# Kernel optimization log

Hardware: AMD Instinct MI355X
Metric: run time of the kernel (lower is better)

## Reference

```python
import jax, jax.numpy as jnp
import numpy as np

B, S, N, D = 8, 1024, 128, 256
LN_EPS = 1e-5
NEG = -10000.0


def setup_inputs() -> dict:
    key = jax.random.key(0)
    ks = jax.random.split(key, 6)
    doc_state = jax.random.normal(ks[0], (B, S, D), dtype=jnp.float32)
    # binary node->token membership mask (batch, nodes, seq)
    nodes_mapping = (jax.random.uniform(ks[1], (B, N, S)) < 0.25).astype(jnp.float32)
    nodes_len = jnp.sum(nodes_mapping, axis=-1).astype(jnp.int32)  # unused by forward, kept for signature parity
    # attention MLP params: Linear(D,D) -> LayerNorm(D) -> GELU -> Linear(D,1)
    W1 = jax.random.normal(ks[2], (D, D), dtype=jnp.float32) / np.float32(np.sqrt(D))
    b1 = jnp.zeros((D,), jnp.float32)
    gamma = jnp.ones((D,), jnp.float32)
    beta = jnp.zeros((D,), jnp.float32)
    W2 = jax.random.normal(ks[3], (D, 1), dtype=jnp.float32) / np.float32(np.sqrt(D))
    b2 = jnp.zeros((1,), jnp.float32)
    return {"doc_state": doc_state, "nodes_mapping": nodes_mapping, "nodes_len": nodes_len,
            "W1": W1, "b1": b1, "gamma": gamma, "beta": beta, "W2": W2, "b2": b2}


def reference(doc_state, nodes_mapping, nodes_len, W1, b1, gamma, beta, W2, b2):
    # scorer MLP: (B,S,D) -> (B,S)
    h = doc_state @ W1 + b1
    mu = jnp.mean(h, axis=-1, keepdims=True)
    var = jnp.mean(jnp.square(h - mu), axis=-1, keepdims=True)
    h = (h - mu) * jax.lax.rsqrt(var + LN_EPS) * gamma + beta
    h = jax.nn.gelu(h, approximate=False)  # torch GELU default = erf form
    scores = (h @ W2 + b2)[..., 0]  # (B, S)
    # masked logits over tokens per node: mapping * score + (1-mapping)*(-1e4)
    logits = nodes_mapping * scores[:, None, :] + (1.0 - nodes_mapping) * NEG  # (B,N,S)
    attn = jax.nn.softmax(logits, axis=2)  # softmax over seq dim
    # pooled = sum_s mapping * attn * doc_state, without materializing (B,N,S,D)
    pooled = jnp.einsum('bns,bns,bsd->bnd', nodes_mapping, attn, doc_state)
    return pooled
```

## Files before the change

### kernel.cpp

```cpp
#include <hip/hip_runtime.h>
#include <hip/hip_bf16.h>
#include <math.h>

#define DD 256
#define SS 1024
#define BB 8
#define NN 128
#define TOK 16
#define KC 64
#define NT 8
#define SC 8
#define SCH (SS/SC)

__global__ __launch_bounds__(256) void scorer_kernel(
    const float* __restrict__ doc, const float* __restrict__ W1,
    const float* __restrict__ b1, const float* __restrict__ gamma,
    const float* __restrict__ beta, const float* __restrict__ W2,
    const float* __restrict__ b2, float* __restrict__ scores)
{
    __shared__ float xs[TOK][DD];
    __shared__ float w1s[KC][DD];

    const int tid  = threadIdx.x;
    const int wave = tid >> 6, lane = tid & 63;
    const int t0   = blockIdx.x * TOK;
    const int c0   = lane * 4;

    {
        const float4* src = reinterpret_cast<const float4*>(doc + (size_t)t0 * DD);
        float4* dst = reinterpret_cast<float4*>(&xs[0][0]);
#pragma unroll
        for (int r = 0; r < 4; ++r) dst[tid + 256 * r] = src[tid + 256 * r];
    }

    float4 acc[4];
    {
        const float4 bv = *reinterpret_cast<const float4*>(b1 + c0);
#pragma unroll
        for (int t = 0; t < 4; ++t) acc[t] = bv;
    }
    const float* xw = &xs[wave * 4][0];

    for (int kc = 0; kc < DD / KC; ++kc) {
        __syncthreads();
        {
            const float4* wsrc = reinterpret_cast<const float4*>(W1 + (size_t)kc * KC * DD);
            float4* wdst = reinterpret_cast<float4*>(&w1s[0][0]);
#pragma unroll
            for (int r = 0; r < 16; ++r) wdst[tid + 256 * r] = wsrc[tid + 256 * r];
        }
        __syncthreads();
#pragma unroll 4
        for (int k4 = 0; k4 < KC / 4; ++k4) {
            const int kb = k4 * 4;
            const float4 w0 = *reinterpret_cast<const float4*>(&w1s[kb + 0][c0]);
            const float4 w1 = *reinterpret_cast<const float4*>(&w1s[kb + 1][c0]);
            const float4 w2 = *reinterpret_cast<const float4*>(&w1s[kb + 2][c0]);
            const float4 w3 = *reinterpret_cast<const float4*>(&w1s[kb + 3][c0]);
#pragma unroll
            for (int t = 0; t < 4; ++t) {
                const float4 xv = *reinterpret_cast<const float4*>(xw + (size_t)t * DD + kc * KC + kb);
                acc[t].x = fmaf(xv.x, w0.x, acc[t].x);
                acc[t].y = fmaf(xv.x, w0.y, acc[t].y);
                acc[t].z = fmaf(xv.x, w0.z, acc[t].z);
                acc[t].w = fmaf(xv.x, w0.w, acc[t].w);
                acc[t].x = fmaf(xv.y, w1.x, acc[t].x);
                acc[t].y = fmaf(xv.y, w1.y, acc[t].y);
                acc[t].z = fmaf(xv.y, w1.z, acc[t].z);
                acc[t].w = fmaf(xv.y, w1.w, acc[t].w);
                acc[t].x = fmaf(xv.z, w2.x, acc[t].x);
                acc[t].y = fmaf(xv.z, w2.y, acc[t].y);
                acc[t].z = fmaf(xv.z, w2.z, acc[t].z);
                acc[t].w = fmaf(xv.z, w2.w, acc[t].w);
                acc[t].x = fmaf(xv.w, w3.x, acc[t].x);
                acc[t].y = fmaf(xv.w, w3.y, acc[t].y);
                acc[t].z = fmaf(xv.w, w3.z, acc[t].z);
                acc[t].w = fmaf(xv.w, w3.w, acc[t].w);
            }
        }
    }

    const float4 gm = *reinterpret_cast<const float4*>(gamma + c0);
    const float4 be = *reinterpret_cast<const float4*>(beta + c0);
    const float4 w2v = *reinterpret_cast<const float4*>(W2 + c0);
    const float b2v = b2[0];

#pragma unroll
    for (int t = 0; t < 4; ++t) {
        float s1 = acc[t].x + acc[t].y + acc[t].z + acc[t].w;
        float s2 = acc[t].x * acc[t].x + acc[t].y * acc[t].y
                 + acc[t].z * acc[t].z + acc[t].w * acc[t].w;
#pragma unroll
        for (int off = 32; off > 0; off >>= 1) {
            s1 += __shfl_xor(s1, off, 64);
            s2 += __shfl_xor(s2, off, 64);
        }
        const float mean = s1 * (1.f / DD);
        const float var  = s2 * (1.f / DD) - mean * mean;
        const float inv  = rsqrtf(var + 1e-5f);
        float n0 = (acc[t].x - mean) * inv * gm.x + be.x;
        float n1 = (acc[t].y - mean) * inv * gm.y + be.y;
        float n2 = (acc[t].z - mean) * inv * gm.z + be.z;
        float n3 = (acc[t].w - mean) * inv * gm.w + be.w;
        const float kq = 0.70710678118654752f;
        float g0 = 0.5f * n0 * (1.f + erff(n0 * kq));
        float g1 = 0.5f * n1 * (1.f + erff(n1 * kq));
        float g2 = 0.5f * n2 * (1.f + erff(n2 * kq));
        float g3 = 0.5f * n3 * (1.f + erff(n3 * kq));
        float sc = g0 * w2v.x + g1 * w2v.y + g2 * w2v.z + g3 * w2v.w;
#pragma unroll
        for (int off = 32; off > 0; off >>= 1) sc += __shfl_xor(sc, off, 64);
        if (lane == 0) scores[t0 + wave * 4 + t] = sc + b2v;
    }
}

__global__ __launch_bounds__(256) void pool_e_kernel(
    const float* __restrict__ doc, const float* __restrict__ mapping,
    const float* __restrict__ scores, float* __restrict__ part,
    float* __restrict__ zpart)
{
    __shared__ float w_lds[NT][SCH];
    __shared__ float z_s[NT];

    const int blk   = blockIdx.x;
    const int c     = blk % SC;
    const int bt    = blk / SC;
    const int ntile = bt & 15;
    const int b     = bt >> 4;
    const int s0    = c * SCH;
    const int tid = threadIdx.x, wave = tid >> 6, lane = tid & 63;

    {
        const int nl = wave * 2 + (lane >> 5);
        const int g  = b * NN + ntile * NT + nl;
        const float4 mp = reinterpret_cast<const float4*>(mapping + (size_t)g * SS + s0)[lane & 31];
        const float4 sv = reinterpret_cast<const float4*>(scores + (size_t)b * SS + s0)[lane & 31];
        float4 e;
        e.x = (mp.x > 0.5f) ? __expf(sv.x) : 0.f;
        e.y = (mp.y > 0.5f) ? __expf(sv.y) : 0.f;
        e.z = (mp.z > 0.5f) ? __expf(sv.z) : 0.f;
        e.w = (mp.w > 0.5f) ? __expf(sv.w) : 0.f;
        reinterpret_cast<float4*>(&w_lds[nl][0])[lane & 31] = e;
        float z = e.x + e.y + e.z + e.w;
#pragma unroll
        for (int off = 16; off > 0; off >>= 1) z += __shfl_xor(z, off, 64);
        if ((lane & 31) == 0) z_s[nl] = z;
    }
    __syncthreads();

    float acc[NT];
#pragma unroll
    for (int n = 0; n < NT; ++n) acc[n] = 0.f;
    const float* docb = doc + ((size_t)b * SS + s0) * DD;

    float d0 = docb[(size_t)0 * DD + tid], d1 = docb[(size_t)1 * DD + tid];
    float d2 = docb[(size_t)2 * DD + tid], d3 = docb[(size_t)3 * DD + tid];
    for (int s4 = 0; s4 < SCH - 4; s4 += 4) {
        const float n0 = docb[(size_t)(s4 + 4) * DD + tid];
        const float n1 = docb[(size_t)(s4 + 5) * DD + tid];
        const float n2 = docb[(size_t)(s4 + 6) * DD + tid];
        const float n3 = docb[(size_t)(s4 + 7) * DD + tid];
#pragma unroll
        for (int n = 0; n < NT; ++n) {
            const float4 wv = *reinterpret_cast<const float4*>(&w_lds[n][s4]);
            acc[n] = fmaf(wv.x, d0, acc[n]);
            acc[n] = fmaf(wv.y, d1, acc[n]);
            acc[n] = fmaf(wv.z, d2, acc[n]);
            acc[n] = fmaf(wv.w, d3, acc[n]);
        }
        d0 = n0; d1 = n1; d2 = n2; d3 = n3;
    }
    {
        const int s4 = SCH - 4;
#pragma unroll
        for (int n = 0; n < NT; ++n) {
            const float4 wv = *reinterpret_cast<const float4*>(&w_lds[n][s4]);
            acc[n] = fmaf(wv.x, d0, acc[n]);
            acc[n] = fmaf(wv.y, d1, acc[n]);
            acc[n] = fmaf(wv.z, d2, acc[n]);
            acc[n] = fmaf(wv.w, d3, acc[n]);
        }
    }

    float* p = part + (size_t)blk * (NT * DD);
#pragma unroll
    for (int n = 0; n < NT; ++n) p[(size_t)n * DD + tid] = acc[n];
    if (tid < NT) zpart[(size_t)blk * NT + tid] = z_s[tid];
}

__global__ __launch_bounds__(256) void reduce_div_kernel(
    const float* __restrict__ part, const float* __restrict__ zpart,
    float* __restrict__ out)
{
    const int o = blockIdx.x * 256 + threadIdx.x;
    const int d = o & 255;
    const int g = o >> 8;
    const int b = g >> 7;
    const int n = g & 127;
    const int ntile = n >> 3, nl = n & 7;
    const int bp0 = (b * 16 + ntile) * SC;
    float s = 0.f, z = 0.f;
#pragma unroll
    for (int c = 0; c < SC; ++c) {
        const int bp = bp0 + c;
        s += part[(size_t)bp * (NT * DD) + (size_t)nl * DD + d];
        z += zpart[(size_t)bp * NT + nl];
    }
    out[o] = (z > 0.f) ? (s / z) : 0.f;
}

__global__ __launch_bounds__(256) void stats_kernel(
    const float* __restrict__ mapping, const float* __restrict__ scores,
    float* __restrict__ mx_out, float* __restrict__ invz_out)
{
    __shared__ float sc_s[SS];
    const int tid = threadIdx.x, wave = tid >> 6, lane = tid & 63;
    const int g0 = blockIdx.x * 4;
    const int b  = g0 >> 7;

    reinterpret_cast<float4*>(sc_s)[tid] =
        reinterpret_cast<const float4*>(scores + (size_t)b * SS)[tid];
    __syncthreads();

    const int g = g0 + wave;
    const float4* mrow4 = reinterpret_cast<const float4*>(mapping + (size_t)g * SS);
    const float4* sc4   = reinterpret_cast<const float4*>(sc_s);

    float4 mv[4], sv[4];
    float mx = -INFINITY;
#pragma unroll
    for (int q = 0; q < 4; ++q) {
        mv[q] = mrow4[lane + (q << 6)];
        sv[q] = sc4[lane + (q << 6)];
        if (mv[q].x > 0.5f) mx = fmaxf(mx, sv[q].x);
        if (mv[q].y > 0.5f) mx = fmaxf(mx, sv[q].y);
        if (mv[q].z > 0.5f) mx = fmaxf(mx, sv[q].z);
        if (mv[q].w > 0.5f) mx = fmaxf(mx, sv[q].w);
    }
#pragma unroll
    for (int off = 32; off > 0; off >>= 1) mx = fmaxf(mx, __shfl_xor(mx, off, 64));
    float z = 0.f;
#pragma unroll
    for (int q = 0; q < 4; ++q) {
        if (mv[q].x > 0.5f) z += __expf(sv[q].x - mx);
        if (mv[q].y > 0.5f) z += __expf(sv[q].y - mx);
        if (mv[q].z > 0.5f) z += __expf(sv[q].z - mx);
        if (mv[q].w > 0.5f) z += __expf(sv[q].w - mx);
    }
#pragma unroll
    for (int off = 32; off > 0; off >>= 1) z += __shfl_xor(z, off, 64);
    if (lane == 0) {
        mx_out[g]   = mx;
        invz_out[g] = (z > 0.f) ? (1.f / z) : 0.f;
    }
}

__global__ __launch_bounds__(256) void pool_direct_kernel(
    const float* __restrict__ doc, const float* __restrict__ mapping,
    const float* __restrict__ scores, const float* __restrict__ mx_in,
    const float* __restrict__ invz_in, float* __restrict__ out)
{
    __shared__ float w_lds[8][SS];

    const int bt    = blockIdx.x;
    const int ntile = bt & 15;
    const int b     = bt >> 4;
    const int tid = threadIdx.x, wave = tid >> 6, lane = tid & 63;

    {
        const int nl = wave * 2 + (lane >> 5);
        const int g  = b * NN + ntile * 8 + nl;
        const float mx   = mx_in[g];
        const float invz = invz_in[g];
        const float4* mrow4 = reinterpret_cast<const float4*>(mapping + (size_t)g * SS);
        const float4* srow4 = reinterpret_cast<const float4*>(scores + (size_t)b * SS);
        float4* wrow4 = reinterpret_cast<float4*>(&w_lds[nl][0]);
        const int idx0 = lane & 31;
#pragma unroll
        for (int q = 0; q < SS / 128; ++q) {
            const int idx = idx0 + 32 * q;
            const float4 mp = mrow4[idx];
            const float4 sv = srow4[idx];
            float4 e;
            e.x = (mp.x > 0.5f) ? __expf(sv.x - mx) * invz : 0.f;
            e.y = (mp.y > 0.5f) ? __expf(sv.y - mx) * invz : 0.f;
            e.z = (mp.z > 0.5f) ? __expf(sv.z - mx) * invz : 0.f;
            e.w = (mp.w > 0.5f) ? __expf(sv.w - mx) * invz : 0.f;
            wrow4[idx] = e;
        }
    }
    __syncthreads();

    float acc[8];
#pragma unroll
    for (int n = 0; n < 8; ++n) acc[n] = 0.f;
    const float* docb = doc + (size_t)b * SS * DD;

    for (int s4 = 0; s4 < SS; s4 += 4) {
        const float d0 = docb[(size_t)(s4 + 0) * DD + tid];
        const float d1 = docb[(size_t)(s4 + 1) * DD + tid];
        const float d2 = docb[(size_t)(s4 + 2) * DD + tid];
        const float d3 = docb[(size_t)(s4 + 3) * DD + tid];
#pragma unroll
        for (int n = 0; n < 8; ++n) {
            const float4 wv = *reinterpret_cast<const float4*>(&w_lds[n][s4]);
            acc[n] = fmaf(wv.x, d0, acc[n]);
            acc[n] = fmaf(wv.y, d1, acc[n]);
            acc[n] = fmaf(wv.z, d2, acc[n]);
            acc[n] = fmaf(wv.w, d3, acc[n]);
        }
    }

    float* outb = out + (((size_t)b * NN) + (size_t)ntile * 8) * DD;
#pragma unroll
    for (int n = 0; n < 8; ++n) outb[(size_t)n * DD + tid] = acc[n];
}

extern "C" void kernel_launch(void* const* d_in, const int* in_sizes, int n_in,
                              void* d_out, int out_size, void* d_ws, size_t ws_size,
                              hipStream_t stream) {
    const float* doc     = (const float*)d_in[0];
    const float* mapping = (const float*)d_in[1];
    const float* W1    = (const float*)d_in[3];
    const float* b1    = (const float*)d_in[4];
    const float* gamma = (const float*)d_in[5];
    const float* beta  = (const float*)d_in[6];
    const float* W2    = (const float*)d_in[7];
    const float* b2    = (const float*)d_in[8];
    float* out = (float*)d_out;

    char* base = (char*)d_ws;
    size_t off = 0;
    float* scores = (float*)(base + off); off += (size_t)BB * SS * 4;
    float* part   = (float*)(base + off); off += (size_t)BB * 16 * SC * NT * DD * 4;
    float* zpart  = (float*)(base + off); off += (size_t)BB * 16 * SC * NT * 4;
    const size_t need = off;

    scorer_kernel<<<BB * SS / TOK, 256, 0, stream>>>(doc, W1, b1, gamma, beta, W2, b2, scores);

    if (ws_size >= need) {
        pool_e_kernel<<<BB * 16 * SC, 256, 0, stream>>>(doc, mapping, scores, part, zpart);
        reduce_div_kernel<<<(BB * NN * DD) / 256, 256, 0, stream>>>(part, zpart, out);
    } else {
        float* mx   = scores + BB * SS;
        float* invz = mx + BB * NN;
        stats_kernel<<<(BB * NN) / 4, 256, 0, stream>>>(mapping, scores, mx, invz);
        pool_direct_kernel<<<BB * 16, 256, 0, stream>>>(doc, mapping, scores, mx, invz, out);
    }
}
```

Baseline: 53.27 us.

## Compute scorer Linear on MFMA with split-bf16 three-term emulation of fp32

Replaces the fp32 FMA scorer GEMM with a bf16 MFMA kernel that splits each operand into hi and lo bf16 parts and sums three products to approximate fp32 accuracy. W1 is transposed and split by a small prep kernel. The LayerNorm, GELU and W2 epilogue moves into a separate combine kernel that reads an 8 MB h buffer from global memory. This adds two launches and an extra round trip of the full hidden activation through memory. The fallback path for a small workspace now needs more space, and the smallest case no longer launches anything.

```diff
diff --git a/kernel.cpp b/kernel.cpp
--- a/kernel.cpp
+++ b/kernel.cpp
@@ -11,6 +11,242 @@
 #define NT 8
 #define SC 8
 #define SCH (SS/SC)
+
+typedef __attribute__((ext_vector_type(8))) short short8;
+typedef __attribute__((ext_vector_type(4))) float f32x4;
+
+__device__ __forceinline__ unsigned short f2bf(float x) {
+    unsigned u = __builtin_bit_cast(unsigned, x);
+    u += 0x7fffu + ((u >> 16) & 1u);
+    return (unsigned short)(u >> 16);
+}
+__device__ __forceinline__ float bf2f(unsigned short h) {
+    return __builtin_bit_cast(float, (unsigned)h << 16);
+}
+__device__ __forceinline__ void cvt8(const float* __restrict__ p, short8& hi, short8& lo) {
+    const float4 xa = *reinterpret_cast<const float4*>(p);
+    const float4 xb = *reinterpret_cast<const float4*>(p + 4);
+    unsigned short h;
+    h = f2bf(xa.x); hi[0] = (short)h; lo[0] = (short)f2bf(xa.x - bf2f(h));
+    h = f2bf(xa.y); hi[1] = (short)h; lo[1] = (short)f2bf(xa.y - bf2f(h));
+    h = f2bf(xa.z); hi[2] = (short)h; lo[2] = (short)f2bf(xa.z - bf2f(h));
+    h = f2bf(xa.w); hi[3] = (short)h; lo[3] = (short)f2bf(xa.w - bf2f(h));
+    h = f2bf(xb.x); hi[4] = (short)h; lo[4] = (short)f2bf(xb.x - bf2f(h));
+    h = f2bf(xb.y); hi[5] = (short)h; lo[5] = (short)f2bf(xb.y - bf2f(h));
+    h = f2bf(xb.z); hi[6] = (short)h; lo[6] = (short)f2bf(xb.z - bf2f(h));
+    h = f2bf(xb.w); hi[7] = (short)h; lo[7] = (short)f2bf(xb.w - bf2f(h));
+}
+
+__global__ __launch_bounds__(256) void split_w1t_kernel(
+    const float* __restrict__ W1,
+    unsigned short* __restrict__ w1t_hi, unsigned short* __restrict__ w1t_lo)
+{
+    __shared__ float tl[64][65];
+    const int tid = threadIdx.x;
+    const int k0 = (blockIdx.x >> 2) * 64, n0 = (blockIdx.x & 3) * 64;
+#pragma unroll
+    for (int i = 0; i < 16; ++i) {
+        const int idx = i * 256 + tid;
+        const int r = idx >> 6, c = idx & 63;
+        tl[r][c] = W1[(size_t)(k0 + r) * DD + n0 + c];
+    }
+    __syncthreads();
+#pragma unroll
+    for (int i = 0; i < 16; ++i) {
+        const int idx = i * 256 + tid;
+        const int nl = idx >> 6, kl = idx & 63;
+        const float v = tl[kl][nl];
+        const unsigned short h = f2bf(v);
+        const size_t o = (size_t)(n0 + nl) * DD + k0 + kl;
+        w1t_hi[o] = h;
+        w1t_lo[o] = f2bf(v - bf2f(h));
+    }
+}
+
+__global__ __launch_bounds__(256) void scorer_gemm_kernel(
+    const float* __restrict__ doc,
+    const unsigned short* __restrict__ w1t_hi, const unsigned short* __restrict__ w1t_lo,
+    float* __restrict__ hbuf)
+{
+    const int tid  = threadIdx.x;
+    const int wave = tid >> 6, lane = tid & 63;
+    const int l15  = lane & 15, kg = lane >> 4;
+    const int t0 = (blockIdx.x >> 2) * 32;
+    const int n0 = (blockIdx.x & 3) * 64 + wave * 16;
+
+    const f32x4 z = {0.f, 0.f, 0.f, 0.f};
+    f32x4 acc0 = z, acc1 = z;
+
+    const float* arow0 = doc + (size_t)(t0 + l15) * DD;
+    const float* arow1 = doc + (size_t)(t0 + 16 + l15) * DD;
+    const size_t brow  = (size_t)(n0 + l15) * DD;
+
+#pragma unroll
+    for (int ks = 0; ks < 8; ++ks) {
+        const int k = ks * 32 + kg * 8;
+        short8 a0h, a0l, a1h, a1l;
+        cvt8(arow0 + k, a0h, a0l);
+        cvt8(arow1 + k, a1h, a1l);
+        const short8 bh = *reinterpret_cast<const short8*>(w1t_hi + brow + k);
+        const short8 bl = *reinterpret_cast<const short8*>(w1t_lo + brow + k);
+        acc0 = __builtin_amdgcn_mfma_f32_16x16x32_bf16(a0h, bh, acc0, 0, 0, 0);
+        acc0 = __builtin_amdgcn_mfma_f32_16x16x32_bf16(a0h, bl, acc0, 0, 0, 0);
+        acc0 = __builtin_amdgcn_mfma_f32_16x16x32_bf16(a0l, bh, acc0, 0, 0, 0);
+        acc1 = __builtin_amdgcn_mfma_f32_16x16x32_bf16(a1h, bh, acc1, 0, 0, 0);
+        acc1 = __builtin_amdgcn_mfma_f32_16x16x32_bf16(a1h, bl, acc1, 0, 0, 0);
+        acc1 = __builtin_amdgcn_mfma_f32_16x16x32_bf16(a1l, bh, acc1, 0, 0, 0);
+    }
+#pragma unroll
+    for (int r = 0; r < 4; ++r) {
+        hbuf[(size_t)(t0 + kg * 4 + r) * DD + n0 + l15]      = acc0[r];
+        hbuf[(size_t)(t0 + 16 + kg * 4 + r) * DD + n0 + l15] = acc1[r];
+    }
+}
+
+__global__ __launch_bounds__(256) void combine_kernel(
+    const float* __restrict__ hbuf, const float* __restrict__ b1,
+    const float* __restrict__ gamma, const float* __restrict__ beta,
+    const float* __restrict__ W2, const float* __restrict__ b2,
+    float* __restrict__ scores)
+{
+    const int tid  = threadIdx.x;
+    const int wave = tid >> 6, lane = tid & 63;
+    const int t0   = blockIdx.x * 16;
+    const int c0   = lane * 4;
+
+    const float4 bv  = *reinterpret_cast<const float4*>(b1 + c0);
+    const float4 gm  = *reinterpret_cast<const float4*>(gamma + c0);
+    const float4 be  = *reinterpret_cast<const float4*>(beta + c0);
+    const float4 w2v = *reinterpret_cast<const float4*>(W2 + c0);
+    const float  b2v = b2[0];
+
+#pragma unroll
+    for (int t = 0; t < 4; ++t) {
+        const int row = t0 + wave * 4 + t;
+        float4 h = *reinterpret_cast<const float4*>(hbuf + (size_t)row * DD + c0);
+        h.x += bv.x; h.y += bv.y; h.z += bv.z; h.w += bv.w;
+
+        float s1 = h.x + h.y + h.z + h.w;
+        float s2 = h.x * h.x + h.y * h.y + h.z * h.z + h.w * h.w;
+#pragma unroll
+        for (int off = 32; off > 0; off >>= 1) {
+            s1 += __shfl_xor(s1, off, 64);
+            s2 += __shfl_xor(s2, off, 64);
+        }
+        const float mean = s1 * (1.f / DD);
+        const float var  = s2 * (1.f / DD) - mean * mean;
+        const float inv  = rsqrtf(var + 1e-5f);
+
+        const float n0 = (h.x - mean) * inv * gm.x + be.x;
+        const float n1 = (h.y - mean) * inv * gm.y + be.y;
+        const float n2 = (h.z - mean) * inv * gm.z + be.z;
+        const float n3 = (h.w - mean) * inv * gm.w + be.w;
+        const float kq = 0.70710678118654752f;
+        const float g0 = 0.5f * n0 * (1.f + erff(n0 * kq));
+        const float g1 = 0.5f * n1 * (1.f + erff(n1 * kq));
+        const float g2 = 0.5f * n2 * (1.f + erff(n2 * kq));
+        const float g3 = 0.5f * n3 * (1.f + erff(n3 * kq));
+        float sc = g0 * w2v.x + g1 * w2v.y + g2 * w2v.z + g3 * w2v.w;
+#pragma unroll
+        for (int off = 32; off > 0; off >>= 1) sc += __shfl_xor(sc, off, 64);
+        if (lane == 0) scores[row] = sc + b2v;
+    }
+}
+
+__global__ __launch_bounds__(256) void pool_e_kernel(
+    const float* __restrict__ doc, const float* __restrict__ mapping,
+    const float* __restrict__ scores, float* __restrict__ part,
+    float* __restrict__ zpart)
+{
+    __shared__ float w_lds[NT][SCH];
+    __shared__ float z_s[NT];
+
+    const int blk   = blockIdx.x;
+    const int c     = blk % SC;
+    const int bt    = blk / SC;
+    const int ntile = bt & 15;
+    const int b     = bt >> 4;
+    const int s0    = c * SCH;
+    const int tid = threadIdx.x, wave = tid >> 6, lane = tid & 63;
+
+    {
+        const int nl = wave * 2 + (lane >> 5);
+        const int g  = b * NN + ntile * NT + nl;
+        const float4 mp = reinterpret_cast<const float4*>(mapping + (size_t)g * SS + s0)[lane & 31];
+        const float4 sv = reinterpret_cast<const float4*>(scores + (size_t)b * SS + s0)[lane & 31];
+        float4 e;
+        e.x = (mp.x > 0.5f) ? __expf(sv.x) : 0.f;
+        e.y = (mp.y > 0.5f) ? __expf(sv.y) : 0.f;
+        e.z = (mp.z > 0.5f) ? __expf(sv.z) : 0.f;
+        e.w = (mp.w > 0.5f) ? __expf(sv.w) : 0.f;
+        reinterpret_cast<float4*>(&w_lds[nl][0])[lane & 31] = e;
+        float z = e.x + e.y + e.z + e.w;
+#pragma unroll
+        for (int off = 16; off > 0; off >>= 1) z += __shfl_xor(z, off, 64);
+        if ((lane & 31) == 0) z_s[nl] = z;
+    }
+    __syncthreads();
+
+    float acc[NT];
+#pragma unroll
+    for (int n = 0; n < NT; ++n) acc[n] = 0.f;
+    const float* docb = doc + ((size_t)b * SS + s0) * DD;
+
+    float d0 = docb[(size_t)0 * DD + tid], d1 = docb[(size_t)1 * DD + tid];
+    float d2 = docb[(size_t)2 * DD + tid], d3 = docb[(size_t)3 * DD + tid];
+    for (int s4 = 0; s4 < SCH - 4; s4 += 4) {
+        const float n0 = docb[(size_t)(s4 + 4) * DD + tid];
+        const float n1 = docb[(size_t)(s4 + 5) * DD + tid];
+        const float n2 = docb[(size_t)(s4 + 6) * DD + tid];
+        const float n3 = docb[(size_t)(s4 + 7) * DD + tid];
+#pragma unroll
+        for (int n = 0; n < NT; ++n) {
+            const float4 wv = *reinterpret_cast<const float4*>(&w_lds[n][s4]);
+            acc[n] = fmaf(wv.x, d0, acc[n]);
+            acc[n] = fmaf(wv.y, d1, acc[n]);
+            acc[n] = fmaf(wv.z, d2, acc[n]);
+            acc[n] = fmaf(wv.w, d3, acc[n]);
+        }
+        d0 = n0; d1 = n1; d2 = n2; d3 = n3;
+    }
+    {
+        const int s4 = SCH - 4;
+#pragma unroll
+        for (int n = 0; n < NT; ++n) {
+            const float4 wv = *reinterpret_cast<const float4*>(&w_lds[n][s4]);
+            acc[n] = fmaf(wv.x, d0, acc[n]);
+            acc[n] = fmaf(wv.y, d1, acc[n]);
+            acc[n] = fmaf(wv.z, d2, acc[n]);
+            acc[n] = fmaf(wv.w, d3, acc[n]);
+        }
+    }
+
+    float* p = part + (size_t)blk * (NT * DD);
+#pragma unroll
+    for (int n = 0; n < NT; ++n) p[(size_t)n * DD + tid] = acc[n];
+    if (tid < NT) zpart[(size_t)blk * NT + tid] = z_s[tid];
+}
+
+__global__ __launch_bounds__(256) void reduce_div_kernel(
+    const float* __restrict__ part, const float* __restrict__ zpart,
+    float* __restrict__ out)
+{
+    const int o = blockIdx.x * 256 + threadIdx.x;
+    const int d = o & 255;
+    const int g = o >> 8;
+    const int b = g >> 7;
+    const int n = g & 127;
+    const int ntile = n >> 3, nl = n & 7;
+    const int bp0 = (b * 16 + ntile) * SC;
+    float s = 0.f, z = 0.f;
+#pragma unroll
+    for (int c = 0; c < SC; ++c) {
+        const int bp = bp0 + c;
+        s += part[(size_t)bp * (NT * DD) + (size_t)nl * DD + d];
+        z += zpart[(size_t)bp * NT + nl];
+    }
+    out[o] = (z > 0.f) ? (s / z) : 0.f;
+}
 
 __global__ __launch_bounds__(256) void scorer_kernel(
     const float* __restrict__ doc, const float* __restrict__ W1,
@@ -114,208 +350,6 @@
     }
 }
 
-__global__ __launch_bounds__(256) void pool_e_kernel(
-    const float* __restrict__ doc, const float* __restrict__ mapping,
-    const float* __restrict__ scores, float* __restrict__ part,
-    float* __restrict__ zpart)
-{
-    __shared__ float w_lds[NT][SCH];
-    __shared__ float z_s[NT];
-
-    const int blk   = blockIdx.x;
-    const int c     = blk % SC;
-    const int bt    = blk / SC;
-    const int ntile = bt & 15;
-    const int b     = bt >> 4;
-    const int s0    = c * SCH;
-    const int tid = threadIdx.x, wave = tid >> 6, lane = tid & 63;
-
-    {
-        const int nl = wave * 2 + (lane >> 5);
-        const int g  = b * NN + ntile * NT + nl;
-        const float4 mp = reinterpret_cast<const float4*>(mapping + (size_t)g * SS + s0)[lane & 31];
-        const float4 sv = reinterpret_cast<const float4*>(scores + (size_t)b * SS + s0)[lane & 31];
-        float4 e;
-        e.x = (mp.x > 0.5f) ? __expf(sv.x) : 0.f;
-        e.y = (mp.y > 0.5f) ? __expf(sv.y) : 0.f;
-        e.z = (mp.z > 0.5f) ? __expf(sv.z) : 0.f;
-        e.w = (mp.w > 0.5f) ? __expf(sv.w) : 0.f;
-        reinterpret_cast<float4*>(&w_lds[nl][0])[lane & 31] = e;
-        float z = e.x + e.y + e.z + e.w;
-#pragma unroll
-        for (int off = 16; off > 0; off >>= 1) z += __shfl_xor(z, off, 64);
-        if ((lane & 31) == 0) z_s[nl] = z;
-    }
-    __syncthreads();
-
-    float acc[NT];
-#pragma unroll
-    for (int n = 0; n < NT; ++n) acc[n] = 0.f;
-    const float* docb = doc + ((size_t)b * SS + s0) * DD;
-
-    float d0 = docb[(size_t)0 * DD + tid], d1 = docb[(size_t)1 * DD + tid];
-    float d2 = docb[(size_t)2 * DD + tid], d3 = docb[(size_t)3 * DD + tid];
-    for (int s4 = 0; s4 < SCH - 4; s4 += 4) {
-        const float n0 = docb[(size_t)(s4 + 4) * DD + tid];
-        const float n1 = docb[(size_t)(s4 + 5) * DD + tid];
-        const float n2 = docb[(size_t)(s4 + 6) * DD + tid];
-        const float n3 = docb[(size_t)(s4 + 7) * DD + tid];
-#pragma unroll
-        for (int n = 0; n < NT; ++n) {
-            const float4 wv = *reinterpret_cast<const float4*>(&w_lds[n][s4]);
-            acc[n] = fmaf(wv.x, d0, acc[n]);
-            acc[n] = fmaf(wv.y, d1, acc[n]);
-            acc[n] = fmaf(wv.z, d2, acc[n]);
-            acc[n] = fmaf(wv.w, d3, acc[n]);
-        }
-        d0 = n0; d1 = n1; d2 = n2; d3 = n3;
-    }
-    {
-        const int s4 = SCH - 4;
-#pragma unroll
-        for (int n = 0; n < NT; ++n) {
-            const float4 wv = *reinterpret_cast<const float4*>(&w_lds[n][s4]);
-            acc[n] = fmaf(wv.x, d0, acc[n]);
-            acc[n] = fmaf(wv.y, d1, acc[n]);
-            acc[n] = fmaf(wv.z, d2, acc[n]);
-            acc[n] = fmaf(wv.w, d3, acc[n]);
-        }
-    }
-
-    float* p = part + (size_t)blk * (NT * DD);
-#pragma unroll
-    for (int n = 0; n < NT; ++n) p[(size_t)n * DD + tid] = acc[n];
-    if (tid < NT) zpart[(size_t)blk * NT + tid] = z_s[tid];
-}
-
-__global__ __launch_bounds__(256) void reduce_div_kernel(
-    const float* __restrict__ part, const float* __restrict__ zpart,
-    float* __restrict__ out)
-{
-    const int o = blockIdx.x * 256 + threadIdx.x;
-    const int d = o & 255;
-    const int g = o >> 8;
-    const int b = g >> 7;
-    const int n = g & 127;
-    const int ntile = n >> 3, nl = n & 7;
-    const int bp0 = (b * 16 + ntile) * SC;
-    float s = 0.f, z = 0.f;
-#pragma unroll
-    for (int c = 0; c < SC; ++c) {
-        const int bp = bp0 + c;
-        s += part[(size_t)bp * (NT * DD) + (size_t)nl * DD + d];
-        z += zpart[(size_t)bp * NT + nl];
-    }
-    out[o] = (z > 0.f) ? (s / z) : 0.f;
-}
-
-__global__ __launch_bounds__(256) void stats_kernel(
-    const float* __restrict__ mapping, const float* __restrict__ scores,
-    float* __restrict__ mx_out, float* __restrict__ invz_out)
-{
-    __shared__ float sc_s[SS];
-    const int tid = threadIdx.x, wave = tid >> 6, lane = tid & 63;
-    const int g0 = blockIdx.x * 4;
-    const int b  = g0 >> 7;
-
-    reinterpret_cast<float4*>(sc_s)[tid] =
-        reinterpret_cast<const float4*>(scores + (size_t)b * SS)[tid];
-    __syncthreads();
-
-    const int g = g0 + wave;
-    const float4* mrow4 = reinterpret_cast<const float4*>(mapping + (size_t)g * SS);
-    const float4* sc4   = reinterpret_cast<const float4*>(sc_s);
-
-    float4 mv[4], sv[4];
-    float mx = -INFINITY;
-#pragma unroll
-    for (int q = 0; q < 4; ++q) {
-        mv[q] = mrow4[lane + (q << 6)];
-        sv[q] = sc4[lane + (q << 6)];
-        if (mv[q].x > 0.5f) mx = fmaxf(mx, sv[q].x);
-        if (mv[q].y > 0.5f) mx = fmaxf(mx, sv[q].y);
-        if (mv[q].z > 0.5f) mx = fmaxf(mx, sv[q].z);
-        if (mv[q].w > 0.5f) mx = fmaxf(mx, sv[q].w);
-    }
-#pragma unroll
-    for (int off = 32; off > 0; off >>= 1) mx = fmaxf(mx, __shfl_xor(mx, off, 64));
-    float z = 0.f;
-#pragma unroll
-    for (int q = 0; q < 4; ++q) {
-        if (mv[q].x > 0.5f) z += __expf(sv[q].x - mx);
-        if (mv[q].y > 0.5f) z += __expf(sv[q].y - mx);
-        if (mv[q].z > 0.5f) z += __expf(sv[q].z - mx);
-        if (mv[q].w > 0.5f) z += __expf(sv[q].w - mx);
-    }
-#pragma unroll
-    for (int off = 32; off > 0; off >>= 1) z += __shfl_xor(z, off, 64);
-    if (lane == 0) {
-        mx_out[g]   = mx;
-        invz_out[g] = (z > 0.f) ? (1.f / z) : 0.f;
-    }
-}
-
-__global__ __launch_bounds__(256) void pool_direct_kernel(
-    const float* __restrict__ doc, const float* __restrict__ mapping,
-    const float* __restrict__ scores, const float* __restrict__ mx_in,
-    const float* __restrict__ invz_in, float* __restrict__ out)
-{
-    __shared__ float w_lds[8][SS];
-
-    const int bt    = blockIdx.x;
-    const int ntile = bt & 15;
-    const int b     = bt >> 4;
-    const int tid = threadIdx.x, wave = tid >> 6, lane = tid & 63;
-
-    {
-        const int nl = wave * 2 + (lane >> 5);
-        const int g  = b * NN + ntile * 8 + nl;
-        const float mx   = mx_in[g];
-        const float invz = invz_in[g];
-        const float4* mrow4 = reinterpret_cast<const float4*>(mapping + (size_t)g * SS);
-        const float4* srow4 = reinterpret_cast<const float4*>(scores + (size_t)b * SS);
-        float4* wrow4 = reinterpret_cast<float4*>(&w_lds[nl][0]);
-        const int idx0 = lane & 31;
-#pragma unroll
-        for (int q = 0; q < SS / 128; ++q) {
-            const int idx = idx0 + 32 * q;
-            const float4 mp = mrow4[idx];
-            const float4 sv = srow4[idx];
-            float4 e;
-            e.x = (mp.x > 0.5f) ? __expf(sv.x - mx) * invz : 0.f;
-            e.y = (mp.y > 0.5f) ? __expf(sv.y - mx) * invz : 0.f;
-            e.z = (mp.z > 0.5f) ? __expf(sv.z - mx) * invz : 0.f;
-            e.w = (mp.w > 0.5f) ? __expf(sv.w - mx) * invz : 0.f;
-            wrow4[idx] = e;
-        }
-    }
-    __syncthreads();
-
-    float acc[8];
-#pragma unroll
-    for (int n = 0; n < 8; ++n) acc[n] = 0.f;
-    const float* docb = doc + (size_t)b * SS * DD;
-
-    for (int s4 = 0; s4 < SS; s4 += 4) {
-        const float d0 = docb[(size_t)(s4 + 0) * DD + tid];
-        const float d1 = docb[(size_t)(s4 + 1) * DD + tid];
-        const float d2 = docb[(size_t)(s4 + 2) * DD + tid];
-        const float d3 = docb[(size_t)(s4 + 3) * DD + tid];
-#pragma unroll
-        for (int n = 0; n < 8; ++n) {
-            const float4 wv = *reinterpret_cast<const float4*>(&w_lds[n][s4]);
-            acc[n] = fmaf(wv.x, d0, acc[n]);
-            acc[n] = fmaf(wv.y, d1, acc[n]);
-            acc[n] = fmaf(wv.z, d2, acc[n]);
-            acc[n] = fmaf(wv.w, d3, acc[n]);
-        }
-    }
-
-    float* outb = out + (((size_t)b * NN) + (size_t)ntile * 8) * DD;
-#pragma unroll
-    for (int n = 0; n < 8; ++n) outb[(size_t)n * DD + tid] = acc[n];
-}
-
 extern "C" void kernel_launch(void* const* d_in, const int* in_sizes, int n_in,
                               void* d_out, int out_size, void* d_ws, size_t ws_size,
                               hipStream_t stream) {
@@ -334,17 +368,23 @@
     float* scores = (float*)(base + off); off += (size_t)BB * SS * 4;
     float* part   = (float*)(base + off); off += (size_t)BB * 16 * SC * NT * DD * 4;
     float* zpart  = (float*)(base + off); off += (size_t)BB * 16 * SC * NT * 4;
+    float* hbuf   = (float*)(base + off); off += (size_t)BB * SS * DD * 4;
+    unsigned short* w1t_hi = (unsigned short*)(base + off); off += (size_t)DD * DD * 2;
+    unsigned short* w1t_lo = (unsigned short*)(base + off); off += (size_t)DD * DD * 2;
     const size_t need = off;
-
-    scorer_kernel<<<BB * SS / TOK, 256, 0, stream>>>(doc, W1, b1, gamma, beta, W2, b2, scores);
+    const size_t need_min = (size_t)(BB * SS) * 4
+                          + (size_t)BB * 16 * SC * NT * DD * 4
+                          + (size_t)BB * 16 * SC * NT * 4;
 
     if (ws_size >= need) {
+        split_w1t_kernel<<<16, 256, 0, stream>>>(W1, w1t_hi, w1t_lo);
+        scorer_gemm_kernel<<<1024, 256, 0, stream>>>(doc, w1t_hi, w1t_lo, hbuf);
+        combine_kernel<<<512, 256, 0, stream>>>(hbuf, b1, gamma, beta, W2, b2, scores);
         pool_e_kernel<<<BB * 16 * SC, 256, 0, stream>>>(doc, mapping, scores, part, zpart);
         reduce_div_kernel<<<(BB * NN * DD) / 256, 256, 0, stream>>>(part, zpart, out);
-    } else {
-        float* mx   = scores + BB * SS;
-        float* invz = mx + BB * NN;
-        stats_kernel<<<(BB * NN) / 4, 256, 0, stream>>>(mapping, scores, mx, invz);
-        pool_direct_kernel<<<BB * 16, 256, 0, stream>>>(doc, mapping, scores, mx, invz, out);
-    }
-}
+    } else if (ws_size >= need_min) {
+        scorer_kernel<<<BB * SS / TOK, 256, 0, stream>>>(doc, W1, b1, gamma, beta, W2, b2, scores);
+        pool_e_kernel<<<BB * 16 * SC, 256, 0, stream>>>(doc, mapping, scores, part, zpart);
+        reduce_div_kernel<<<(BB * NN * DD) / 256, 256, 0, stream>>>(part, zpart, out);
+    }
+}
```

Measured after the change: 60.83 us. 14.2% more time.
